# Optimization experiments

Measured on AMD Instinct MI355X. Metric: run time of the kernel, lower is better.

Reference implementation:

```python
import jax, jax.numpy as jnp
import numpy as np

E, NH, G = 2048, 16, 4
HD = E // NH          # head_dim = 128
KV = E // G           # kv proj width = 512 == G * HD
B, S = 2, 2048


def setup_inputs() -> dict:
    key = jax.random.key(0)
    ks = jax.random.split(key, 7)
    s = lambda n: 1.0 / np.sqrt(n)
    return {
        "query": jax.random.normal(ks[0], (B, S, E), jnp.float32),
        "key_in": jax.random.normal(ks[1], (B, S, E), jnp.float32),
        "value": jax.random.normal(ks[2], (B, S, E), jnp.float32),
        "Wq": jax.random.normal(ks[3], (E, E), jnp.float32) * s(E),
        "bq": jnp.zeros((E,), jnp.float32),
        "Wk": jax.random.normal(ks[4], (E, KV), jnp.float32) * s(E),
        "bk": jnp.zeros((KV,), jnp.float32),
        "Wv": jax.random.normal(ks[5], (E, KV), jnp.float32) * s(E),
        "bv": jnp.zeros((KV,), jnp.float32),
        "Wo": jax.random.normal(ks[6], (E, E), jnp.float32) * s(E),
        "bo": jnp.zeros((E,), jnp.float32),
    }


def reference(query, key_in, value, Wq, bq, Wk, bk, Wv, bv, Wo, bo):
    b, s, _ = query.shape
    scale = HD ** -0.5
    # projections
    q = (query @ Wq + bq).reshape(b, s, NH, HD).transpose(0, 2, 1, 3)   # [B,NH,S,HD]
    k = (key_in @ Wk + bk).reshape(b, s, G, HD).transpose(0, 2, 1, 3)   # [B,G,S,HD]
    v = (value @ Wv + bv).reshape(b, s, G, HD).transpose(0, 2, 1, 3)    # [B,G,S,HD]
    # grouped-query attention: each KV head serves NH//G query heads
    qg = q.reshape(b, G, NH // G, s, HD)                                # [B,G,NH/G,S,HD]
    scores = jnp.einsum('bgqsh,bgth->bgqst', qg, k) * scale             # [B,G,NH/G,S,S]
    w = jax.nn.softmax(scores, axis=-1)
    out = jnp.einsum('bgqst,bgth->bgqsh', w, v)                         # [B,G,NH/G,S,HD]
    out = out.reshape(b, NH, s, HD).transpose(0, 2, 1, 3).reshape(b, s, E)
    return out @ Wo + bo
```

## Files before the change

kernel.cpp:

```cpp
#include <hip/hip_runtime.h>
#include <hip/hip_bf16.h>

#define E_ 2048
#define S_ 2048
#define B_ 2
#define BS_ 4096
#define KV_ 512
#define NH_ 16
#define G_ 4
#define HD_ 128
#define QK_SCALE 0.08838834764831845f
#define LOG2E_ 1.4426950408889634f

typedef __attribute__((ext_vector_type(8))) short short8;
typedef __attribute__((ext_vector_type(4))) float floatx4;
typedef __attribute__((ext_vector_type(4))) unsigned short ushort4_;

static __device__ __forceinline__ unsigned short f2bf(float f) {
  unsigned int u = __builtin_bit_cast(unsigned int, f);
  u += 0x7fffu + ((u >> 16) & 1u);
  return (unsigned short)(u >> 16);
}

static __device__ __forceinline__ unsigned int cvt_pk_bf16(float lo, float hi) {
  unsigned int r;
  asm("v_cvt_pk_bf16_f32 %0, %1, %2" : "=v"(r) : "v"(lo), "v"(hi));
  return r;
}

static __device__ __forceinline__ void gld16(const void* g, void* l) {
  __builtin_amdgcn_global_load_lds(
      (const __attribute__((address_space(1))) unsigned int*)g,
      (__attribute__((address_space(3))) unsigned int*)l, 16, 0, 0);
}

__global__ __launch_bounds__(256) void k_prep(
    const float* __restrict__ q, const float* __restrict__ k, const float* __restrict__ v,
    unsigned short* __restrict__ xq, unsigned short* __restrict__ xk,
    unsigned short* __restrict__ xv,
    const float* __restrict__ Wq, unsigned short* __restrict__ WqT,
    const float* __restrict__ Wk, unsigned short* __restrict__ WkT,
    const float* __restrict__ Wv, unsigned short* __restrict__ WvT,
    const float* __restrict__ Wo, unsigned short* __restrict__ WoT) {
  __shared__ float ts[32][33];
  int bid = blockIdx.x;
  if (bid < 24576) {
    int which = bid >> 13;
    int i = (bid & 8191) * 256 + threadIdx.x;
    const float* in = (which == 0) ? q : (which == 1) ? k : v;
    unsigned short* out = (which == 0) ? xq : (which == 1) ? xk : xv;
    float4 vv = reinterpret_cast<const float4*>(in)[i];
    ushort4_ o;
    o.x = f2bf(vv.x); o.y = f2bf(vv.y); o.z = f2bf(vv.z); o.w = f2bf(vv.w);
    reinterpret_cast<ushort4_*>(out)[i] = o;
    return;
  }
  int t = bid - 24576;
  const float* in; unsigned short* out; int N; int rem;
  if (t < 4096)      { in = Wq; out = WqT; N = 2048; rem = t; }
  else if (t < 5120) { in = Wk; out = WkT; N = 512;  rem = t - 4096; }
  else if (t < 6144) { in = Wv; out = WvT; N = 512;  rem = t - 5120; }
  else               { in = Wo; out = WoT; N = 2048; rem = t - 6144; }
  const int K = 2048;
  int nx = N >> 5;
  int bx = rem % nx, by = rem / nx;
  int tx = threadIdx.x & 31, ty = threadIdx.x >> 5;
  int n0 = bx * 32, k0 = by * 32;
#pragma unroll
  for (int i = 0; i < 4; ++i)
    ts[ty + i * 8][tx] = in[(size_t)(k0 + ty + i * 8) * N + n0 + tx];
  __syncthreads();
#pragma unroll
  for (int i = 0; i < 4; ++i)
    out[(size_t)(n0 + ty + i * 8) * K + k0 + tx] = f2bf(ts[tx][ty + i * 8]);
}

template <bool OUT_F32>
static __device__ __forceinline__ void gemm_bt_tile(
    const unsigned short* __restrict__ A, const unsigned short* __restrict__ Bt,
    const float* __restrict__ bias, bool rowBias, void* __restrict__ C,
    int N, int K, float scale, int bx, int by,
    unsigned short* As, unsigned short* Bs) {
  const int tid = threadIdx.x;
  const int w = tid >> 6;
  const int lhi = (tid >> 4) & 3;
  const int llo = tid & 15;
  const int wr = w >> 1, wc = w & 1;
  const size_t brow = (size_t)by * 128, bcol = (size_t)bx * 128;

  auto stage = [&](int k0, int bufi) {
#pragma unroll
    for (int i = 0; i < 2; ++i) {
      int o = i * 256 + tid;
      gld16(A + (brow + (o >> 2)) * K + k0 + (o & 3) * 8,
            As + bufi * 4096 + (size_t)(i * 256 + w * 64) * 8);
      gld16(Bt + (bcol + (o >> 2)) * K + k0 + (o & 3) * 8,
            Bs + bufi * 4096 + (size_t)(i * 256 + w * 64) * 8);
    }
  };

  floatx4 acc[4][4];
#pragma unroll
  for (int i = 0; i < 4; ++i)
#pragma unroll
    for (int j = 0; j < 4; ++j)
      acc[i][j] = (floatx4){0.f, 0.f, 0.f, 0.f};

  stage(0, 0);
  __syncthreads();
  int buf = 0;
  const int nk = K >> 5;
  for (int t = 0; t < nk; ++t) {
    if (t + 1 < nk) stage((t + 1) * 32, buf ^ 1);
    const unsigned short* Ab = As + buf * 4096;
    const unsigned short* Bb = Bs + buf * 4096;
    short8 a[4], b[4];
#pragma unroll
    for (int f = 0; f < 4; ++f) {
      a[f] = *reinterpret_cast<const short8*>(Ab + (wr * 64 + f * 16 + llo) * 32 + lhi * 8);
      b[f] = *reinterpret_cast<const short8*>(Bb + (wc * 64 + f * 16 + llo) * 32 + lhi * 8);
    }
    __builtin_amdgcn_s_setprio(1);
#pragma unroll
    for (int i = 0; i < 4; ++i)
#pragma unroll
      for (int j = 0; j < 4; ++j)
        acc[i][j] = __builtin_amdgcn_mfma_f32_16x16x32_bf16(a[i], b[j], acc[i][j], 0, 0, 0);
    __builtin_amdgcn_s_setprio(0);
    __syncthreads();
    buf ^= 1;
  }

#pragma unroll
  for (int i = 0; i < 4; ++i) {
#pragma unroll
    for (int j = 0; j < 4; ++j) {
      size_t gr0 = brow + wr * 64 + i * 16 + lhi * 4;
      size_t gc = bcol + wc * 64 + j * 16 + llo;
#pragma unroll
      for (int r = 0; r < 4; ++r) {
        size_t grow = gr0 + r;
        float v = acc[i][j][r];
        v += rowBias ? bias[grow] : bias[gc];
        v *= scale;
        if (OUT_F32)
          ((float*)C)[grow * N + gc] = v;
        else
          ((unsigned short*)C)[grow * N + gc] = f2bf(v);
      }
    }
  }
}

__global__ __launch_bounds__(256) void k_gemm_qkv(
    const unsigned short* __restrict__ xq, const unsigned short* __restrict__ WqT,
    const float* __restrict__ bq, unsigned short* __restrict__ qb,
    const unsigned short* __restrict__ xk, const unsigned short* __restrict__ WkT,
    const float* __restrict__ bk, unsigned short* __restrict__ kb,
    const unsigned short* __restrict__ WvT, const unsigned short* __restrict__ xv,
    const float* __restrict__ bv, unsigned short* __restrict__ vtb) {
  __shared__ __align__(16) unsigned short As[2 * 128 * 32];
  __shared__ __align__(16) unsigned short Bs[2 * 128 * 32];
  int bid = blockIdx.x;
  if (bid < 512) {
    gemm_bt_tile<false>(xq, WqT, bq, false, qb, E_, E_, QK_SCALE * LOG2E_,
                        bid & 15, bid >> 4, As, Bs);
  } else if (bid < 640) {
    int b2 = bid - 512;
    gemm_bt_tile<false>(xk, WkT, bk, false, kb, KV_, E_, 1.0f, b2 & 3, b2 >> 2, As, Bs);
  } else {
    int b2 = bid - 640;
    gemm_bt_tile<false>(WvT, xv, bv, true, vtb, BS_, E_, 1.0f, b2 & 31, b2 >> 5, As, Bs);
  }
}

__global__ __launch_bounds__(256) void k_gemm_o(
    const unsigned short* __restrict__ A, const unsigned short* __restrict__ Bt,
    const float* __restrict__ bias, float* __restrict__ C) {
  __shared__ __align__(16) unsigned short As[2 * 128 * 32];
  __shared__ __align__(16) unsigned short Bs[2 * 128 * 32];
  gemm_bt_tile<true>(A, Bt, bias, false, C, E_, E_, 1.0f,
                     blockIdx.x & 15, blockIdx.x >> 4, As, Bs);
}

__global__ __launch_bounds__(256) void k_attn(
    const unsigned short* __restrict__ qb, const unsigned short* __restrict__ kb,
    const unsigned short* __restrict__ vt, unsigned short* __restrict__ attn) {
  __shared__ __align__(16) unsigned short Ks[2][64 * 128];
  __shared__ __align__(16) unsigned short Vs[2][128 * 64];
  __shared__ __align__(16) unsigned short Ps[4][32 * 64];

  const int tid = threadIdx.x;
  const int w = tid >> 6;
  const int lhi = (tid >> 4) & 3;
  const int llo = tid & 15;
  const int bid = blockIdx.x;
  const int xcd = bid & 7;
  const int b = xcd >> 2, g = xcd & 3;
  const int inner = bid >> 3;
  const int hq = inner & 3, qt = inner >> 2;
  const int h = g * 4 + hq;

  char* PsW = (char*)&Ps[0][0] + w * 4096;

  short8 qf[2][4];
#pragma unroll
  for (int rt = 0; rt < 2; ++rt)
#pragma unroll
    for (int hc = 0; hc < 4; ++hc) {
      int row = qt * 128 + w * 32 + rt * 16 + llo;
      qf[rt][hc] = *reinterpret_cast<const short8*>(
          qb + ((size_t)(b * 2048 + row)) * 2048 + h * 128 + hc * 32 + lhi * 8);
    }

  floatx4 acc[2][8];
#pragma unroll
  for (int rt = 0; rt < 2; ++rt)
#pragma unroll
    for (int dc = 0; dc < 8; ++dc)
      acc[rt][dc] = (floatx4){0.f, 0.f, 0.f, 0.f};
  float m_[2] = {-1e30f, -1e30f};
  float l_[2] = {0.f, 0.f};

  auto stage = [&](int kv0, int buf) {
#pragma unroll
    for (int i = 0; i < 4; ++i) {
      int o = i * 256 + tid;
      int row = o >> 4, gr2 = (o & 15) ^ (row & 7);
      gld16(kb + ((size_t)(b * 2048 + kv0 + row)) * 512 + g * 128 + gr2 * 8,
            &Ks[buf][(size_t)(i * 256 + w * 64) * 8]);
    }
#pragma unroll
    for (int i = 0; i < 4; ++i) {
      int o = i * 256 + tid;
      int row = o >> 3, gr2 = (o & 7) ^ (row & 7);
      gld16(vt + ((size_t)(g * 128 + row)) * 4096 + b * 2048 + kv0 + gr2 * 8,
            &Vs[buf][(size_t)(i * 256 + w * 64) * 8]);
    }
  };

  stage(0, 0);
  __syncthreads();
  int buf = 0;

  for (int t = 0; t < 32; ++t) {
    const int kv0 = t * 64;
    if (t < 31) stage(kv0 + 64, buf ^ 1);

    floatx4 sc[2][4];
#pragma unroll
    for (int rt = 0; rt < 2; ++rt)
#pragma unroll
      for (int c = 0; c < 4; ++c)
        sc[rt][c] = (floatx4){0.f, 0.f, 0.f, 0.f};
    __builtin_amdgcn_s_setprio(1);
#pragma unroll
    for (int c = 0; c < 4; ++c) {
      int krow = c * 16 + llo;
#pragma unroll
      for (int hc = 0; hc < 4; ++hc) {
        int byteoff = krow * 256 + ((hc * 64 + lhi * 16) ^ ((krow & 7) << 4));
        short8 kf = *reinterpret_cast<const short8*>((const char*)&Ks[buf][0] + byteoff);
        sc[0][c] = __builtin_amdgcn_mfma_f32_16x16x32_bf16(kf, qf[0][hc], sc[0][c], 0, 0, 0);
        sc[1][c] = __builtin_amdgcn_mfma_f32_16x16x32_bf16(kf, qf[1][hc], sc[1][c], 0, 0, 0);
      }
    }
    __builtin_amdgcn_s_setprio(0);

#pragma unroll
    for (int rt = 0; rt < 2; ++rt) {
      float pm = sc[rt][0][0];
#pragma unroll
      for (int c = 0; c < 4; ++c)
#pragma unroll
        for (int r = 0; r < 4; ++r) pm = fmaxf(pm, sc[rt][c][r]);
      if (__any(pm > m_[rt] + 8.0f)) {
        float t2 = pm;
        t2 = fmaxf(t2, __shfl_xor(t2, 16));
        t2 = fmaxf(t2, __shfl_xor(t2, 32));
        float m2 = fmaxf(m_[rt], t2);
        float scr = __builtin_amdgcn_exp2f(m_[rt] - m2);
        m_[rt] = m2;
        l_[rt] *= scr;
#pragma unroll
        for (int r = 0; r < 4; ++r) {
          float s_r = __shfl(scr, (tid & 48) | (((tid >> 2) & 12) + r));
#pragma unroll
          for (int dc = 0; dc < 8; ++dc) acc[rt][dc][r] *= s_r;
        }
      }
      float lsum = l_[rt];
#pragma unroll
      for (int c = 0; c < 4; ++c) {
        float e0 = __builtin_amdgcn_exp2f(sc[rt][c][0] - m_[rt]);
        float e1 = __builtin_amdgcn_exp2f(sc[rt][c][1] - m_[rt]);
        float e2 = __builtin_amdgcn_exp2f(sc[rt][c][2] - m_[rt]);
        float e3 = __builtin_amdgcn_exp2f(sc[rt][c][3] - m_[rt]);
        lsum += (e0 + e1) + (e2 + e3);
        uint2 pk;
        pk.x = cvt_pk_bf16(e0, e1);
        pk.y = cvt_pk_bf16(e2, e3);
        int byteoff = (rt * 16 + llo) * 128 + ((c * 32 + lhi * 8) ^ ((llo & 7) << 4));
        *reinterpret_cast<uint2*>(PsW + byteoff) = pk;
      }
      l_[rt] = lsum;
    }

    short8 pf[2][2];
#pragma unroll
    for (int rt = 0; rt < 2; ++rt)
#pragma unroll
      for (int kc = 0; kc < 2; ++kc) {
        int byteoff = (rt * 16 + llo) * 128 + ((kc * 64 + lhi * 16) ^ ((llo & 7) << 4));
        pf[rt][kc] = *reinterpret_cast<const short8*>(PsW + byteoff);
      }
    __builtin_amdgcn_s_setprio(1);
#pragma unroll
    for (int dc = 0; dc < 8; ++dc) {
      int vrow = dc * 16 + llo;
      int bo0 = vrow * 128 + ((lhi * 16) ^ ((vrow & 7) << 4));
      int bo1 = vrow * 128 + ((64 + lhi * 16) ^ ((vrow & 7) << 4));
      short8 vf0 = *reinterpret_cast<const short8*>((const char*)&Vs[buf][0] + bo0);
      short8 vf1 = *reinterpret_cast<const short8*>((const char*)&Vs[buf][0] + bo1);
      acc[0][dc] = __builtin_amdgcn_mfma_f32_16x16x32_bf16(pf[0][0], vf0, acc[0][dc], 0, 0, 0);
      acc[1][dc] = __builtin_amdgcn_mfma_f32_16x16x32_bf16(pf[1][0], vf0, acc[1][dc], 0, 0, 0);
      acc[0][dc] = __builtin_amdgcn_mfma_f32_16x16x32_bf16(pf[0][1], vf1, acc[0][dc], 0, 0, 0);
      acc[1][dc] = __builtin_amdgcn_mfma_f32_16x16x32_bf16(pf[1][1], vf1, acc[1][dc], 0, 0, 0);
    }
    __builtin_amdgcn_s_setprio(0);
    __syncthreads();
    buf ^= 1;
  }

#pragma unroll
  for (int rt = 0; rt < 2; ++rt) {
    float t2 = l_[rt];
    t2 += __shfl_xor(t2, 16);
    t2 += __shfl_xor(t2, 32);
    float linv = 1.0f / t2;
    float lr[4];
#pragma unroll
    for (int r = 0; r < 4; ++r)
      lr[r] = __shfl(linv, (tid & 48) | (((tid >> 2) & 12) + r));
#pragma unroll
    for (int dc = 0; dc < 8; ++dc)
#pragma unroll
      for (int r = 0; r < 4; ++r) {
        int row = qt * 128 + w * 32 + rt * 16 + lhi * 4 + r;
        float v = acc[rt][dc][r] * lr[r];
        attn[((size_t)(b * 2048 + row)) * 2048 + h * 128 + dc * 16 + llo] = f2bf(v);
      }
  }
}

extern "C" void kernel_launch(void* const* d_in, const int* in_sizes, int n_in,
                              void* d_out, int out_size, void* d_ws, size_t ws_size,
                              hipStream_t stream) {
  const float* query  = (const float*)d_in[0];
  const float* key_in = (const float*)d_in[1];
  const float* value  = (const float*)d_in[2];
  const float* Wq = (const float*)d_in[3];
  const float* bq = (const float*)d_in[4];
  const float* Wk = (const float*)d_in[5];
  const float* bk = (const float*)d_in[6];
  const float* Wv = (const float*)d_in[7];
  const float* bv = (const float*)d_in[8];
  const float* Wo = (const float*)d_in[9];
  const float* bo = (const float*)d_in[10];
  float* out = (float*)d_out;

  char* ws = (char*)d_ws;
  size_t off = 0;
  auto alloc = [&](size_t bytes) {
    char* p = ws + off;
    off += (bytes + 255) & ~(size_t)255;
    return p;
  };
  unsigned short* xq   = (unsigned short*)alloc((size_t)BS_ * E_ * 2);
  unsigned short* xk   = (unsigned short*)alloc((size_t)BS_ * E_ * 2);
  unsigned short* xv   = (unsigned short*)alloc((size_t)BS_ * E_ * 2);
  unsigned short* WqT  = (unsigned short*)alloc((size_t)E_ * E_ * 2);
  unsigned short* WkT  = (unsigned short*)alloc((size_t)KV_ * E_ * 2);
  unsigned short* WvT  = (unsigned short*)alloc((size_t)KV_ * E_ * 2);
  unsigned short* WoT  = (unsigned short*)alloc((size_t)E_ * E_ * 2);
  unsigned short* qb   = (unsigned short*)alloc((size_t)BS_ * E_ * 2);
  unsigned short* kb   = (unsigned short*)alloc((size_t)BS_ * KV_ * 2);
  unsigned short* vtb  = (unsigned short*)alloc((size_t)KV_ * BS_ * 2);
  unsigned short* attb = (unsigned short*)alloc((size_t)BS_ * E_ * 2);

  k_prep<<<34816, 256, 0, stream>>>(query, key_in, value, xq, xk, xv,
                                    Wq, WqT, Wk, WkT, Wv, WvT, Wo, WoT);
  k_gemm_qkv<<<768, 256, 0, stream>>>(xq, WqT, bq, qb, xk, WkT, bk, kb,
                                      WvT, xv, bv, vtb);
  k_attn<<<B_ * NH_ * (S_ / 128), 256, 0, stream>>>(qb, kb, vtb, attb);
  k_gemm_o<<<512, 256, 0, stream>>>(attb, WoT, bo, out);
}
```

Before: 255.7 us.

## Load K fragments directly into registers and remap GEMM tile order per XCD

In the attention kernel, the shared-memory staging of K is removed. Each wave now loads its K MFMA fragments straight from global memory into registers, prefetching the next tile after the PV step. This cuts LDS use and LDS reads, and launch_bounds(256,2) is added to allow two blocks per CU. The GEMM kernels also remap block IDs so that consecutive blocks on the same XCD cover neighbouring tiles for better L2 locality. The trade-offs are extra register pressure from holding 16 short8 K fragments, redundant global reads of K across waves, and exposed global-load latency.

```diff
diff --git a/kernel.cpp b/kernel.cpp
--- a/kernel.cpp
+++ b/kernel.cpp
@@ -163,14 +163,17 @@
   __shared__ __align__(16) unsigned short Bs[2 * 128 * 32];
   int bid = blockIdx.x;
   if (bid < 512) {
+    int cm = (bid & 7) * 64 + (bid >> 3);
     gemm_bt_tile<false>(xq, WqT, bq, false, qb, E_, E_, QK_SCALE * LOG2E_,
-                        bid & 15, bid >> 4, As, Bs);
+                        cm >> 5, cm & 31, As, Bs);
   } else if (bid < 640) {
-    int b2 = bid - 512;
-    gemm_bt_tile<false>(xk, WkT, bk, false, kb, KV_, E_, 1.0f, b2 & 3, b2 >> 2, As, Bs);
+    int u = bid - 512;
+    int cm = (u & 7) * 16 + (u >> 3);
+    gemm_bt_tile<false>(xk, WkT, bk, false, kb, KV_, E_, 1.0f, cm >> 5, cm & 31, As, Bs);
   } else {
-    int b2 = bid - 640;
-    gemm_bt_tile<false>(WvT, xv, bv, true, vtb, BS_, E_, 1.0f, b2 & 31, b2 >> 5, As, Bs);
+    int u = bid - 640;
+    int cm = (u & 7) * 16 + (u >> 3);
+    gemm_bt_tile<false>(WvT, xv, bv, true, vtb, BS_, E_, 1.0f, cm >> 2, cm & 3, As, Bs);
   }
 }
 
@@ -179,14 +182,13 @@
     const float* __restrict__ bias, float* __restrict__ C) {
   __shared__ __align__(16) unsigned short As[2 * 128 * 32];
   __shared__ __align__(16) unsigned short Bs[2 * 128 * 32];
-  gemm_bt_tile<true>(A, Bt, bias, false, C, E_, E_, 1.0f,
-                     blockIdx.x & 15, blockIdx.x >> 4, As, Bs);
-}
-
-__global__ __launch_bounds__(256) void k_attn(
+  int cm = (blockIdx.x & 7) * 64 + (blockIdx.x >> 3);
+  gemm_bt_tile<true>(A, Bt, bias, false, C, E_, E_, 1.0f, cm >> 5, cm & 31, As, Bs);
+}
+
+__global__ __launch_bounds__(256, 2) void k_attn(
     const unsigned short* __restrict__ qb, const unsigned short* __restrict__ kb,
     const unsigned short* __restrict__ vt, unsigned short* __restrict__ attn) {
-  __shared__ __align__(16) unsigned short Ks[2][64 * 128];
   __shared__ __align__(16) unsigned short Vs[2][128 * 64];
   __shared__ __align__(16) unsigned short Ps[4][32 * 64];
 
@@ -213,6 +215,8 @@
           qb + ((size_t)(b * 2048 + row)) * 2048 + h * 128 + hc * 32 + lhi * 8);
     }
 
+  const unsigned short* kbase = kb + (size_t)(b * 2048) * 512 + g * 128;
+
   floatx4 acc[2][8];
 #pragma unroll
   for (int rt = 0; rt < 2; ++rt)
@@ -222,14 +226,7 @@
   float m_[2] = {-1e30f, -1e30f};
   float l_[2] = {0.f, 0.f};
 
-  auto stage = [&](int kv0, int buf) {
-#pragma unroll
-    for (int i = 0; i < 4; ++i) {
-      int o = i * 256 + tid;
-      int row = o >> 4, gr2 = (o & 15) ^ (row & 7);
-      gld16(kb + ((size_t)(b * 2048 + kv0 + row)) * 512 + g * 128 + gr2 * 8,
-            &Ks[buf][(size_t)(i * 256 + w * 64) * 8]);
-    }
+  auto stageV = [&](int kv0, int buf) {
 #pragma unroll
     for (int i = 0; i < 4; ++i) {
       int o = i * 256 + tid;
@@ -239,13 +236,24 @@
     }
   };
 
-  stage(0, 0);
+  short8 kf[4][4];
+  auto loadK = [&](int kv0) {
+#pragma unroll
+    for (int c = 0; c < 4; ++c)
+#pragma unroll
+      for (int hc = 0; hc < 4; ++hc)
+        kf[c][hc] = *reinterpret_cast<const short8*>(
+            kbase + (size_t)(kv0 + c * 16 + llo) * 512 + hc * 32 + lhi * 8);
+  };
+
+  stageV(0, 0);
+  loadK(0);
   __syncthreads();
   int buf = 0;
 
   for (int t = 0; t < 32; ++t) {
     const int kv0 = t * 64;
-    if (t < 31) stage(kv0 + 64, buf ^ 1);
+    if (t < 31) stageV(kv0 + 64, buf ^ 1);
 
     floatx4 sc[2][4];
 #pragma unroll
@@ -255,16 +263,12 @@
         sc[rt][c] = (floatx4){0.f, 0.f, 0.f, 0.f};
     __builtin_amdgcn_s_setprio(1);
 #pragma unroll
-    for (int c = 0; c < 4; ++c) {
-      int krow = c * 16 + llo;
+    for (int c = 0; c < 4; ++c)
 #pragma unroll
       for (int hc = 0; hc < 4; ++hc) {
-        int byteoff = krow * 256 + ((hc * 64 + lhi * 16) ^ ((krow & 7) << 4));
-        short8 kf = *reinterpret_cast<const short8*>((const char*)&Ks[buf][0] + byteoff);
-        sc[0][c] = __builtin_amdgcn_mfma_f32_16x16x32_bf16(kf, qf[0][hc], sc[0][c], 0, 0, 0);
-        sc[1][c] = __builtin_amdgcn_mfma_f32_16x16x32_bf16(kf, qf[1][hc], sc[1][c], 0, 0, 0);
-      }
-    }
+        sc[0][c] = __builtin_amdgcn_mfma_f32_16x16x32_bf16(kf[c][hc], qf[0][hc], sc[0][c], 0, 0, 0);
+        sc[1][c] = __builtin_amdgcn_mfma_f32_16x16x32_bf16(kf[c][hc], qf[1][hc], sc[1][c], 0, 0, 0);
+      }
     __builtin_amdgcn_s_setprio(0);
 
 #pragma unroll
@@ -328,6 +332,8 @@
       acc[1][dc] = __builtin_amdgcn_mfma_f32_16x16x32_bf16(pf[1][1], vf1, acc[1][dc], 0, 0, 0);
     }
     __builtin_amdgcn_s_setprio(0);
+
+    loadK((t < 31) ? kv0 + 64 : 0);
     __syncthreads();
     buf ^= 1;
   }
```

After: 294.1 us. +15.0%, slower.
